# Kernel tuning notes

Hardware: AMD Instinct MI355X
Metric: run time of the kernel (lower is better)

The kernel has to match this reference:

```python
import jax, jax.numpy as jnp
import numpy as np

N = 50000
E = 800000
NODE_DIM = 128
EDGE_DIM = 64


def leaky_relu(x, slope=0.2):
    return jnp.where(x >= 0, x, slope * x)


def setup_inputs() -> dict:
    key = jax.random.key(0)
    ks = jax.random.split(key, 12)
    node_feats = jax.random.normal(ks[0], (N, NODE_DIM), dtype=jnp.float32)
    edge_index = jax.random.randint(ks[1], (2, E), 0, N, dtype=jnp.int64)
    edge_feats = jax.random.normal(ks[2], (E, EDGE_DIM), dtype=jnp.float32)
    # msg_mlp: Linear(node+edge -> node), LeakyReLU(0.2), Linear(node -> node)
    s1 = 1.0 / np.sqrt(NODE_DIM + EDGE_DIM)
    s2 = 1.0 / np.sqrt(NODE_DIM)
    s3 = 1.0 / np.sqrt(2 * NODE_DIM)
    msg_w1 = jax.random.uniform(ks[3], (NODE_DIM + EDGE_DIM, NODE_DIM), jnp.float32, -s1, s1)
    msg_b1 = jax.random.uniform(ks[4], (NODE_DIM,), jnp.float32, -s1, s1)
    msg_w2 = jax.random.uniform(ks[5], (NODE_DIM, NODE_DIM), jnp.float32, -s2, s2)
    msg_b2 = jax.random.uniform(ks[6], (NODE_DIM,), jnp.float32, -s2, s2)
    # update_mlp: Linear(2*node -> node), LeakyReLU(0.2), Linear(node -> node)
    upd_w1 = jax.random.uniform(ks[7], (2 * NODE_DIM, NODE_DIM), jnp.float32, -s3, s3)
    upd_b1 = jax.random.uniform(ks[8], (NODE_DIM,), jnp.float32, -s3, s3)
    upd_w2 = jax.random.uniform(ks[9], (NODE_DIM, NODE_DIM), jnp.float32, -s2, s2)
    upd_b2 = jax.random.uniform(ks[10], (NODE_DIM,), jnp.float32, -s2, s2)
    return {
        "node_feats": node_feats,
        "edge_feats": edge_feats,
        "msg_w1": msg_w1, "msg_b1": msg_b1, "msg_w2": msg_w2, "msg_b2": msg_b2,
        "upd_w1": upd_w1, "upd_b1": upd_b1, "upd_w2": upd_w2, "upd_b2": upd_b2,
        "edge_index": edge_index,
    }


def reference(node_feats, edge_feats, msg_w1, msg_b1, msg_w2, msg_b2,
              upd_w1, upd_b1, upd_w2, upd_b2, edge_index):
    src = edge_index[0]
    dst = edge_index[1]
    # gather neighbor features, concat with edge features: (E, node+edge)
    msg_input = jnp.concatenate([node_feats[dst], edge_feats], axis=1)
    h = leaky_relu(msg_input @ msg_w1 + msg_b1)
    messages = h @ msg_w2 + msg_b2                       # (E, node_dim)
    # scatter-add messages to source nodes
    aggregated = jax.ops.segment_sum(messages, src, num_segments=node_feats.shape[0])
    update_input = jnp.concatenate([node_feats, aggregated], axis=1)  # (N, 2*node_dim)
    h2 = leaky_relu(update_input @ upd_w1 + upd_b1)
    return h2 @ upd_w2 + upd_b2                          # (N, node_dim)
```

## Files before the change

### kernel.cpp

```cpp
#include <hip/hip_runtime.h>
#include <hip/hip_bf16.h>

#define NNODES 50000
#define NEDGES 800000
#define NDIM   128
#define EDIM   64
#define K1     192
#define K2     256
#define NB     196
#define TPB_E  4

#define KPA 136
#define KPU 264

typedef __attribute__((ext_vector_type(8))) short bf16x8;
typedef __attribute__((ext_vector_type(4))) short bf16x4;
typedef __attribute__((ext_vector_type(4))) float f32x4;

__device__ inline short f2bf(float f) {
  union { float f; unsigned u; } v; v.f = f;
  unsigned r = v.u + 0x7FFFu + ((v.u >> 16) & 1u);
  return (short)(r >> 16);
}

__device__ inline bf16x4 pack4(float4 v) {
  bf16x4 p;
  p[0] = f2bf(v.x); p[1] = f2bf(v.y); p[2] = f2bf(v.z); p[3] = f2bf(v.w);
  return p;
}

__device__ inline void wg_barrier_lds() {
  asm volatile("s_waitcnt lgkmcnt(0)" ::: "memory");
  __builtin_amdgcn_s_barrier();
  asm volatile("" ::: "memory");
}

__global__ __launch_bounds__(256) void cvt_kernel(const float* __restrict__ src,
                                                  short* __restrict__ dst, int n) {
  int i = (blockIdx.x * 256 + threadIdx.x) * 4;
  if (i < n) {
    float4 v = *(const float4*)(src + i);
    *(bf16x4*)(dst + i) = pack4(v);
  }
}

__global__ __launch_bounds__(256) void wt_all_kernel(const float* __restrict__ w1,
                                                     const float* __restrict__ w2,
                                                     const float* __restrict__ u1,
                                                     const float* __restrict__ u2,
                                                     short* __restrict__ w1t,
                                                     short* __restrict__ w2t,
                                                     short* __restrict__ u1t,
                                                     short* __restrict__ u2t) {
  int i = blockIdx.x * 256 + threadIdx.x;
  const int A0 = K1 * 128;
  const int A1 = A0 + 128 * 128;
  const int A2 = A1 + K2 * 128;
  const int A3 = A2 + 128 * 128;
  if (i < A0) {
    int j = i, k = j >> 7, n = j & 127;
    w1t[n * K1 + k] = f2bf(w1[j]);
  } else if (i < A1) {
    int j = i - A0, k = j >> 7, n = j & 127;
    w2t[n * NDIM + k] = f2bf(w2[j]);
  } else if (i < A2) {
    int j = i - A1, k = j >> 7, n = j & 127;
    u1t[n * K2 + k] = f2bf(u1[j]);
  } else if (i < A3) {
    int j = i - A2, k = j >> 7, n = j & 127;
    u2t[n * NDIM + k] = f2bf(u2[j]);
  }
}

__global__ __launch_bounds__(256) void hist_kernel(const int* __restrict__ eidx,
                                                   int* __restrict__ cnt) {
  int i = blockIdx.x * 256 + threadIdx.x;
  if (i < NEDGES) atomicAdd(&cnt[eidx[i]], 1);
}

__global__ __launch_bounds__(256) void scan_reduce_kernel(const int* __restrict__ cnt,
                                                          int* __restrict__ bsum) {
  __shared__ int sh[256];
  int tid = threadIdx.x;
  int i = blockIdx.x * 256 + tid;
  sh[tid] = (i < NNODES) ? cnt[i] : 0;
  __syncthreads();
#pragma unroll
  for (int off = 128; off > 0; off >>= 1) {
    if (tid < off) sh[tid] += sh[tid + off];
    __syncthreads();
  }
  if (tid == 0) bsum[blockIdx.x] = sh[0];
}

__global__ __launch_bounds__(256) void scan_top_kernel(const int* __restrict__ bsum,
                                                       int* __restrict__ bscan) {
  __shared__ int sh[256];
  int tid = threadIdx.x;
  int v = (tid < NB) ? bsum[tid] : 0;
  sh[tid] = v;
  __syncthreads();
#pragma unroll
  for (int off = 1; off < 256; off <<= 1) {
    int t = (tid >= off) ? sh[tid - off] : 0;
    __syncthreads();
    sh[tid] += t;
    __syncthreads();
  }
  bscan[tid] = sh[tid] - v;
}

__global__ __launch_bounds__(256) void scan_down_kernel(int* __restrict__ cnt,
                                                        const int* __restrict__ bscan,
                                                        int* __restrict__ row_ptr) {
  __shared__ int sh[256];
  int tid = threadIdx.x;
  int i = blockIdx.x * 256 + tid;
  int v = (i < NNODES) ? cnt[i] : 0;
  sh[tid] = v;
  __syncthreads();
#pragma unroll
  for (int off = 1; off < 256; off <<= 1) {
    int t = (tid >= off) ? sh[tid - off] : 0;
    __syncthreads();
    sh[tid] += t;
    __syncthreads();
  }
  if (i < NNODES) {
    row_ptr[i] = bscan[blockIdx.x] + (sh[tid] - v);
    cnt[i] = 0;
  }
}

__global__ __launch_bounds__(256) void permute_kernel(const int* __restrict__ eidx,
                                                      const int* __restrict__ row_ptr,
                                                      int* __restrict__ cnt,
                                                      int4* __restrict__ s_edges) {
  int e = blockIdx.x * 256 + threadIdx.x;
  if (e < NEDGES) {
    int s = eidx[e];
    int d = eidx[NEDGES + e];
    int pos = row_ptr[s] + atomicAdd(&cnt[s], 1);
    s_edges[pos] = make_int4(s, d, e, 0);
  }
}

__global__ __launch_bounds__(256, 3) void edge_kernel(const short* __restrict__ nf_bf,
                                                      const float* __restrict__ edge_feats,
                                                      const int4* __restrict__ s_edges,
                                                      const short* __restrict__ w1t,
                                                      const float* __restrict__ b1,
                                                      float* __restrict__ hagg) {
  __shared__ __align__(16) short XN[2][64 * 128];
  __shared__ __align__(16) short XE[64 * 64];
  __shared__ int srcs[64];

  const int tid = threadIdx.x;
  const int lane = tid & 63;
  const int wv = tid >> 6;
  const int m16 = lane & 15;
  const int quad = lane >> 4;
  const int r = tid >> 2, q = tid & 3;
  const int rx = r & 7;
  const int mx = m16 & 7;

  const int e0 = blockIdx.x * (64 * TPB_E);

  float bias[2];
#pragma unroll
  for (int nt = 0; nt < 2; ++nt) bias[nt] = b1[wv * 32 + nt * 16 + m16];

  bf16x8 bfrag[6][2];
#pragma unroll
  for (int ks = 0; ks < 6; ++ks)
#pragma unroll
    for (int nt = 0; nt < 2; ++nt)
      bfrag[ks][nt] = *(const bf16x8*)(w1t + (wv * 32 + nt * 16 + m16) * K1 + ks * 32 + quad * 8);

  int4 rec = s_edges[e0 + r];
  bf16x8 pn[4];
  float4 pe[4];
  {
    const bf16x8* np = (const bf16x8*)(nf_bf + (size_t)rec.y * NDIM) + q * 4;
#pragma unroll
    for (int j = 0; j < 4; ++j) pn[j] = np[j];
    const float4* ep = (const float4*)(edge_feats + (size_t)rec.z * EDIM) + q * 4;
#pragma unroll
    for (int j = 0; j < 4; ++j) pe[j] = ep[j];
  }

  for (int t = 0; t < TPB_E; ++t) {
    short* xn = XN[t & 1];

    {
      short* rowp = xn + r * 128;
#pragma unroll
      for (int j = 0; j < 4; ++j)
        *(bf16x8*)(rowp + (((q * 4 + j) ^ rx) << 3)) = pn[j];
      bf16x4 c0 = pack4(pe[0]), c1 = pack4(pe[1]), c2 = pack4(pe[2]), c3 = pack4(pe[3]);
      bf16x8 p0, p1;
      p0[0]=c0[0]; p0[1]=c0[1]; p0[2]=c0[2]; p0[3]=c0[3];
      p0[4]=c1[0]; p0[5]=c1[1]; p0[6]=c1[2]; p0[7]=c1[3];
      p1[0]=c2[0]; p1[1]=c2[1]; p1[2]=c2[2]; p1[3]=c2[3];
      p1[4]=c3[0]; p1[5]=c3[1]; p1[6]=c3[2]; p1[7]=c3[3];
      short* erow = XE + r * 64;
      *(bf16x8*)(erow + (((q * 2 + 0) ^ rx) << 3)) = p0;
      *(bf16x8*)(erow + (((q * 2 + 1) ^ rx) << 3)) = p1;
      if (q == 0) srcs[r] = rec.x;
    }
    __syncthreads();

    if (t + 1 < TPB_E) {
      rec = s_edges[e0 + (t + 1) * 64 + r];
      const bf16x8* np = (const bf16x8*)(nf_bf + (size_t)rec.y * NDIM) + q * 4;
#pragma unroll
      for (int j = 0; j < 4; ++j) pn[j] = np[j];
      const float4* ep = (const float4*)(edge_feats + (size_t)rec.z * EDIM) + q * 4;
#pragma unroll
      for (int j = 0; j < 4; ++j) pe[j] = ep[j];
    }

    f32x4 acc[4][2];
#pragma unroll
    for (int mt = 0; mt < 4; ++mt)
#pragma unroll
      for (int nt = 0; nt < 2; ++nt) acc[mt][nt] = (f32x4){0.f, 0.f, 0.f, 0.f};
#pragma unroll
    for (int ks = 0; ks < 4; ++ks) {
#pragma unroll
      for (int mt = 0; mt < 4; ++mt) {
        bf16x8 a = *(const bf16x8*)(xn + (mt * 16 + m16) * 128 + (((ks * 4 + quad) ^ mx) << 3));
#pragma unroll
        for (int nt = 0; nt < 2; ++nt)
          acc[mt][nt] = __builtin_amdgcn_mfma_f32_16x16x32_bf16(a, bfrag[ks][nt], acc[mt][nt], 0, 0, 0);
      }
    }
#pragma unroll
    for (int ks = 4; ks < 6; ++ks) {
#pragma unroll
      for (int mt = 0; mt < 4; ++mt) {
        bf16x8 a = *(const bf16x8*)(XE + (mt * 16 + m16) * 64 + ((((ks - 4) * 4 + quad) ^ mx) << 3));
#pragma unroll
        for (int nt = 0; nt < 2; ++nt)
          acc[mt][nt] = __builtin_amdgcn_mfma_f32_16x16x32_bf16(a, bfrag[ks][nt], acc[mt][nt], 0, 0, 0);
      }
    }
    wg_barrier_lds();

    float* M = (float*)xn;
#pragma unroll
    for (int h = 0; h < 2; ++h) {
#pragma unroll
      for (int nt = 0; nt < 2; ++nt) {
        const int col = wv * 32 + nt * 16 + m16;
        const float bb = bias[nt];
#pragma unroll
        for (int mt2 = 0; mt2 < 2; ++mt2) {
          const int mt = h * 2 + mt2;
#pragma unroll
          for (int i = 0; i < 4; ++i) {
            float v = acc[mt][nt][i] + bb;
            v = v >= 0.f ? v : 0.2f * v;
            M[(mt2 * 16 + quad * 4 + i) * 128 + col] = v;
          }
        }
      }
      wg_barrier_lds();
      {
        const int c = tid & 127;
        const int lr0 = (tid >> 7) * 16;
        const int g0 = h * 32 + lr0;
        float a = M[lr0 * 128 + c];
        int prev = srcs[g0];
#pragma unroll 4
        for (int rr = 1; rr < 16; ++rr) {
          int s = srcs[g0 + rr];
          float v = M[(lr0 + rr) * 128 + c];
          if (s != prev) {
            atomicAdd(&hagg[(size_t)prev * NDIM + c], a);
            a = v;
            prev = s;
          } else {
            a += v;
          }
        }
        atomicAdd(&hagg[(size_t)prev * NDIM + c], a);
      }
      wg_barrier_lds();
    }
  }
}

__global__ __launch_bounds__(256) void node_kernel(const short* __restrict__ nf_bf,
                                                   const float* __restrict__ hagg,
                                                   const int* __restrict__ degc,
                                                   const short* __restrict__ w2t,
                                                   const float* __restrict__ b2,
                                                   const short* __restrict__ u1t,
                                                   const float* __restrict__ ub1,
                                                   const short* __restrict__ u2t,
                                                   const float* __restrict__ ub2,
                                                   float* __restrict__ out) {
  __shared__ __align__(16) short AGH[32 * KPA];
  __shared__ __align__(16) short XU[32 * KPU];
  __shared__ float degs[32];

  const int tid = threadIdx.x;
  const int n0 = blockIdx.x * 32;

  if (tid < 32) {
    int node = n0 + tid;
    degs[tid] = (node < NNODES) ? (float)degc[node] : 0.f;
  }
  {
    int r = tid >> 3, q = tid & 7;
    int node = n0 + r; if (node >= NNODES) node = NNODES - 1;
    const float4* hp = (const float4*)(hagg + (size_t)node * NDIM) + q * 4;
    const bf16x8* xp = (const bf16x8*)(nf_bf + (size_t)node * NDIM) + q * 2;
    short* ap = AGH + r * KPA + q * 16;
    short* xq = XU + r * KPU + q * 16;
#pragma unroll
    for (int j = 0; j < 4; ++j) *(bf16x4*)(ap + j * 4) = pack4(hp[j]);
#pragma unroll
    for (int j = 0; j < 2; ++j) *(bf16x8*)(xq + j * 8) = xp[j];
  }
  __syncthreads();

  const int lane = tid & 63;
  const int wv = tid >> 6;
  const int m16 = lane & 15;
  const int quad = lane >> 4;

  f32x4 acc[2][2];

#pragma unroll
  for (int mt = 0; mt < 2; ++mt)
#pragma unroll
    for (int nt = 0; nt < 2; ++nt)
      acc[mt][nt] = (f32x4){0.f, 0.f, 0.f, 0.f};
#pragma unroll
  for (int ks = 0; ks < 4; ++ks) {
    const int k0 = ks * 32 + quad * 8;
    bf16x8 b[2];
#pragma unroll
    for (int nt = 0; nt < 2; ++nt) {
      int n = wv * 32 + nt * 16 + m16;
      b[nt] = *(const bf16x8*)(w2t + n * NDIM + k0);
    }
#pragma unroll
    for (int mt = 0; mt < 2; ++mt) {
      bf16x8 a = *(const bf16x8*)(AGH + (mt * 16 + m16) * KPA + k0);
#pragma unroll
      for (int nt = 0; nt < 2; ++nt)
        acc[mt][nt] = __builtin_amdgcn_mfma_f32_16x16x32_bf16(a, b[nt], acc[mt][nt], 0, 0, 0);
    }
  }
#pragma unroll
  for (int nt = 0; nt < 2; ++nt) {
    int col = wv * 32 + nt * 16 + m16;
    float bb = b2[col];
#pragma unroll
    for (int mt = 0; mt < 2; ++mt) {
#pragma unroll
      for (int i = 0; i < 4; ++i) {
        int row = mt * 16 + quad * 4 + i;
        float v = acc[mt][nt][i] + degs[row] * bb;
        XU[row * KPU + NDIM + col] = f2bf(v);
      }
    }
  }
  __syncthreads();

#pragma unroll
  for (int mt = 0; mt < 2; ++mt)
#pragma unroll
    for (int nt = 0; nt < 2; ++nt)
      acc[mt][nt] = (f32x4){0.f, 0.f, 0.f, 0.f};
#pragma unroll
  for (int ks = 0; ks < 8; ++ks) {
    const int k0 = ks * 32 + quad * 8;
    bf16x8 b[2];
#pragma unroll
    for (int nt = 0; nt < 2; ++nt) {
      int n = wv * 32 + nt * 16 + m16;
      b[nt] = *(const bf16x8*)(u1t + n * K2 + k0);
    }
#pragma unroll
    for (int mt = 0; mt < 2; ++mt) {
      bf16x8 a = *(const bf16x8*)(XU + (mt * 16 + m16) * KPU + k0);
#pragma unroll
      for (int nt = 0; nt < 2; ++nt)
        acc[mt][nt] = __builtin_amdgcn_mfma_f32_16x16x32_bf16(a, b[nt], acc[mt][nt], 0, 0, 0);
    }
  }
  __syncthreads();
#pragma unroll
  for (int nt = 0; nt < 2; ++nt) {
    int col = wv * 32 + nt * 16 + m16;
    float bb = ub1[col];
#pragma unroll
    for (int mt = 0; mt < 2; ++mt) {
#pragma unroll
      for (int i = 0; i < 4; ++i) {
        int row = mt * 16 + quad * 4 + i;
        float v = acc[mt][nt][i] + bb;
        v = v >= 0.f ? v : 0.2f * v;
        AGH[row * KPA + col] = f2bf(v);
      }
    }
  }
  __syncthreads();

#pragma unroll
  for (int mt = 0; mt < 2; ++mt)
#pragma unroll
    for (int nt = 0; nt < 2; ++nt)
      acc[mt][nt] = (f32x4){0.f, 0.f, 0.f, 0.f};
#pragma unroll
  for (int ks = 0; ks < 4; ++ks) {
    const int k0 = ks * 32 + quad * 8;
    bf16x8 b[2];
#pragma unroll
    for (int nt = 0; nt < 2; ++nt) {
      int n = wv * 32 + nt * 16 + m16;
      b[nt] = *(const bf16x8*)(u2t + n * NDIM + k0);
    }
#pragma unroll
    for (int mt = 0; mt < 2; ++mt) {
      bf16x8 a = *(const bf16x8*)(AGH + (mt * 16 + m16) * KPA + k0);
#pragma unroll
      for (int nt = 0; nt < 2; ++nt)
        acc[mt][nt] = __builtin_amdgcn_mfma_f32_16x16x32_bf16(a, b[nt], acc[mt][nt], 0, 0, 0);
    }
  }
#pragma unroll
  for (int nt = 0; nt < 2; ++nt) {
    int col = wv * 32 + nt * 16 + m16;
    float bb = ub2[col];
#pragma unroll
    for (int mt = 0; mt < 2; ++mt) {
#pragma unroll
      for (int i = 0; i < 4; ++i) {
        int row = mt * 16 + quad * 4 + i;
        int node = n0 + row;
        if (node < NNODES)
          out[(size_t)node * NDIM + col] = acc[mt][nt][i] + bb;
      }
    }
  }
}

extern "C" void kernel_launch(void* const* d_in, const int* in_sizes, int n_in,
                              void* d_out, int out_size, void* d_ws, size_t ws_size,
                              hipStream_t stream) {
  const float* node_feats = (const float*)d_in[0];
  const float* edge_feats = (const float*)d_in[1];
  const float* msg_w1 = (const float*)d_in[2];
  const float* msg_b1 = (const float*)d_in[3];
  const float* msg_w2 = (const float*)d_in[4];
  const float* msg_b2 = (const float*)d_in[5];
  const float* upd_w1 = (const float*)d_in[6];
  const float* upd_b1 = (const float*)d_in[7];
  const float* upd_w2 = (const float*)d_in[8];
  const float* upd_b2 = (const float*)d_in[9];
  const int* eidx = (const int*)d_in[10];

  float* hagg   = (float*)d_ws;
  int* cnt      = (int*)(hagg + (size_t)NNODES * NDIM);
  int* row_ptr  = cnt + NNODES;
  int* bsum     = row_ptr + NNODES;
  int* bscan    = bsum + 256;
  int4* s_edges = (int4*)(bscan + 256);
  short* w1t    = (short*)(s_edges + NEDGES);
  short* w2t    = w1t + 128 * K1;
  short* u1t    = w2t + 128 * 128;
  short* u2t    = u1t + 128 * K2;
  short* nf_bf  = u2t + 128 * 128;

  hipMemsetAsync(d_ws, 0, (size_t)(NNODES * NDIM + NNODES) * sizeof(float), stream);

  cvt_kernel<<<(NNODES * NDIM / 4 + 255) / 256, 256, 0, stream>>>(node_feats, nf_bf,
                                                                  NNODES * NDIM);
  wt_all_kernel<<<(90112 + 255) / 256, 256, 0, stream>>>(msg_w1, msg_w2, upd_w1, upd_w2,
                                                         w1t, w2t, u1t, u2t);

  hist_kernel<<<NEDGES / 256, 256, 0, stream>>>(eidx, cnt);
  scan_reduce_kernel<<<NB, 256, 0, stream>>>(cnt, bsum);
  scan_top_kernel<<<1, 256, 0, stream>>>(bsum, bscan);
  scan_down_kernel<<<NB, 256, 0, stream>>>(cnt, bscan, row_ptr);
  permute_kernel<<<NEDGES / 256, 256, 0, stream>>>(eidx, row_ptr, cnt, s_edges);

  edge_kernel<<<NEDGES / (64 * TPB_E), 256, 0, stream>>>(nf_bf, edge_feats, s_edges,
                                                         w1t, msg_b1, hagg);
  node_kernel<<<(NNODES + 31) / 32, 256, 0, stream>>>(nf_bf, hagg, cnt,
                                                      w2t, msg_b2, u1t, upd_b1,
                                                      u2t, upd_b2, (float*)d_out);
}
```

Baseline: 507.3 us.

## Merge prep kernels and shrink edge-kernel LDS to raise occupancy

Fuses the node-feature conversion, weight transpose and degree histogram into one prep launch, cutting two kernel launches. The edge kernel drops its double-buffered LDS and reuses a single padded region for inputs and the message staging tile. The padded stride of 130 floats is meant to reduce bank conflicts, and the launch bound is raised to 4 blocks per CU. Each tile now stages all 64 rows at once, with one barrier pair instead of two halves. Losing the double buffer may add serialisation between tiles, and the tighter launch bound may cause register spills.

```diff
diff --git a/kernel.cpp b/kernel.cpp
--- a/kernel.cpp
+++ b/kernel.cpp
@@ -9,6 +9,7 @@
 #define K2     256
 #define NB     196
 #define TPB_E  4
+#define MSTR   130
 
 #define KPA 136
 #define KPU 264
@@ -35,47 +36,46 @@
   asm volatile("" ::: "memory");
 }
 
-__global__ __launch_bounds__(256) void cvt_kernel(const float* __restrict__ src,
-                                                  short* __restrict__ dst, int n) {
-  int i = (blockIdx.x * 256 + threadIdx.x) * 4;
-  if (i < n) {
-    float4 v = *(const float4*)(src + i);
-    *(bf16x4*)(dst + i) = pack4(v);
-  }
-}
-
-__global__ __launch_bounds__(256) void wt_all_kernel(const float* __restrict__ w1,
-                                                     const float* __restrict__ w2,
-                                                     const float* __restrict__ u1,
-                                                     const float* __restrict__ u2,
-                                                     short* __restrict__ w1t,
-                                                     short* __restrict__ w2t,
-                                                     short* __restrict__ u1t,
-                                                     short* __restrict__ u2t) {
-  int i = blockIdx.x * 256 + threadIdx.x;
-  const int A0 = K1 * 128;
-  const int A1 = A0 + 128 * 128;
-  const int A2 = A1 + K2 * 128;
-  const int A3 = A2 + 128 * 128;
-  if (i < A0) {
-    int j = i, k = j >> 7, n = j & 127;
-    w1t[n * K1 + k] = f2bf(w1[j]);
-  } else if (i < A1) {
-    int j = i - A0, k = j >> 7, n = j & 127;
-    w2t[n * NDIM + k] = f2bf(w2[j]);
-  } else if (i < A2) {
-    int j = i - A1, k = j >> 7, n = j & 127;
-    u1t[n * K2 + k] = f2bf(u1[j]);
-  } else if (i < A3) {
-    int j = i - A2, k = j >> 7, n = j & 127;
-    u2t[n * NDIM + k] = f2bf(u2[j]);
-  }
-}
-
-__global__ __launch_bounds__(256) void hist_kernel(const int* __restrict__ eidx,
+__global__ __launch_bounds__(256) void prep_kernel(const float* __restrict__ nf,
+                                                   short* __restrict__ nf_bf,
+                                                   const float* __restrict__ w1,
+                                                   const float* __restrict__ w2,
+                                                   const float* __restrict__ u1,
+                                                   const float* __restrict__ u2,
+                                                   short* __restrict__ w1t,
+                                                   short* __restrict__ w2t,
+                                                   short* __restrict__ u1t,
+                                                   short* __restrict__ u2t,
+                                                   const int* __restrict__ eidx,
                                                    int* __restrict__ cnt) {
-  int i = blockIdx.x * 256 + threadIdx.x;
-  if (i < NEDGES) atomicAdd(&cnt[eidx[i]], 1);
+  const int b = blockIdx.x;
+  const int tid = threadIdx.x;
+  if (b < 6250) {
+    int i = (b * 256 + tid) * 4;
+    float4 v = *(const float4*)(nf + i);
+    *(bf16x4*)(nf_bf + i) = pack4(v);
+  } else if (b < 6602) {
+    int i = (b - 6250) * 256 + tid;
+    const int A0 = K1 * 128;
+    const int A1 = A0 + 128 * 128;
+    const int A2 = A1 + K2 * 128;
+    if (i < A0) {
+      int j = i, k = j >> 7, n = j & 127;
+      w1t[n * K1 + k] = f2bf(w1[j]);
+    } else if (i < A1) {
+      int j = i - A0, k = j >> 7, n = j & 127;
+      w2t[n * NDIM + k] = f2bf(w2[j]);
+    } else if (i < A2) {
+      int j = i - A1, k = j >> 7, n = j & 127;
+      u1t[n * K2 + k] = f2bf(u1[j]);
+    } else {
+      int j = i - A2, k = j >> 7, n = j & 127;
+      u2t[n * NDIM + k] = f2bf(u2[j]);
+    }
+  } else {
+    int e = (b - 6602) * 256 + tid;
+    atomicAdd(&cnt[eidx[e]], 1);
+  }
 }
 
 __global__ __launch_bounds__(256) void scan_reduce_kernel(const int* __restrict__ cnt,
@@ -145,15 +145,18 @@
   }
 }
 
-__global__ __launch_bounds__(256, 3) void edge_kernel(const short* __restrict__ nf_bf,
+__global__ __launch_bounds__(256, 4) void edge_kernel(const short* __restrict__ nf_bf,
                                                       const float* __restrict__ edge_feats,
                                                       const int4* __restrict__ s_edges,
                                                       const short* __restrict__ w1t,
                                                       const float* __restrict__ b1,
                                                       float* __restrict__ hagg) {
-  __shared__ __align__(16) short XN[2][64 * 128];
-  __shared__ __align__(16) short XE[64 * 64];
+  __shared__ __align__(16) char SH[64 * MSTR * 4];
   __shared__ int srcs[64];
+
+  short* X  = (short*)SH;
+  short* XE = (short*)(SH + 16384);
+  float* M  = (float*)SH;
 
   const int tid = threadIdx.x;
   const int lane = tid & 63;
@@ -190,10 +193,8 @@
   }
 
   for (int t = 0; t < TPB_E; ++t) {
-    short* xn = XN[t & 1];
-
     {
-      short* rowp = xn + r * 128;
+      short* rowp = X + r * 128;
 #pragma unroll
       for (int j = 0; j < 4; ++j)
         *(bf16x8*)(rowp + (((q * 4 + j) ^ rx) << 3)) = pn[j];
@@ -229,7 +230,7 @@
     for (int ks = 0; ks < 4; ++ks) {
 #pragma unroll
       for (int mt = 0; mt < 4; ++mt) {
-        bf16x8 a = *(const bf16x8*)(xn + (mt * 16 + m16) * 128 + (((ks * 4 + quad) ^ mx) << 3));
+        bf16x8 a = *(const bf16x8*)(X + (mt * 16 + m16) * 128 + (((ks * 4 + quad) ^ mx) << 3));
 #pragma unroll
         for (int nt = 0; nt < 2; ++nt)
           acc[mt][nt] = __builtin_amdgcn_mfma_f32_16x16x32_bf16(a, bfrag[ks][nt], acc[mt][nt], 0, 0, 0);
@@ -247,35 +248,34 @@
     }
     wg_barrier_lds();
 
-    float* M = (float*)xn;
-#pragma unroll
-    for (int h = 0; h < 2; ++h) {
-#pragma unroll
-      for (int nt = 0; nt < 2; ++nt) {
-        const int col = wv * 32 + nt * 16 + m16;
-        const float bb = bias[nt];
-#pragma unroll
-        for (int mt2 = 0; mt2 < 2; ++mt2) {
-          const int mt = h * 2 + mt2;
-#pragma unroll
-          for (int i = 0; i < 4; ++i) {
-            float v = acc[mt][nt][i] + bb;
-            v = v >= 0.f ? v : 0.2f * v;
-            M[(mt2 * 16 + quad * 4 + i) * 128 + col] = v;
-          }
+#pragma unroll
+    for (int nt = 0; nt < 2; ++nt) {
+      const int col = wv * 32 + nt * 16 + m16;
+      const float bb = bias[nt];
+#pragma unroll
+      for (int mt = 0; mt < 4; ++mt) {
+#pragma unroll
+        for (int i = 0; i < 4; ++i) {
+          float v = acc[mt][nt][i] + bb;
+          v = v >= 0.f ? v : 0.2f * v;
+          M[(mt * 16 + quad * 4 + i) * MSTR + col] = v;
         }
       }
-      wg_barrier_lds();
-      {
-        const int c = tid & 127;
-        const int lr0 = (tid >> 7) * 16;
-        const int g0 = h * 32 + lr0;
-        float a = M[lr0 * 128 + c];
-        int prev = srcs[g0];
+    }
+    wg_barrier_lds();
+
+    {
+      const int c = tid & 127;
+      const int sb = (tid >> 7) * 16;
+#pragma unroll
+      for (int half = 0; half < 2; ++half) {
+        const int lr0 = sb + half * 32;
+        float a = M[lr0 * MSTR + c];
+        int prev = srcs[lr0];
 #pragma unroll 4
         for (int rr = 1; rr < 16; ++rr) {
-          int s = srcs[g0 + rr];
-          float v = M[(lr0 + rr) * 128 + c];
+          int s = srcs[lr0 + rr];
+          float v = M[(lr0 + rr) * MSTR + c];
           if (s != prev) {
             atomicAdd(&hagg[(size_t)prev * NDIM + c], a);
             a = v;
@@ -286,8 +286,8 @@
         }
         atomicAdd(&hagg[(size_t)prev * NDIM + c], a);
       }
-      wg_barrier_lds();
-    }
+    }
+    wg_barrier_lds();
   }
 }
 
@@ -479,12 +479,10 @@
 
   hipMemsetAsync(d_ws, 0, (size_t)(NNODES * NDIM + NNODES) * sizeof(float), stream);
 
-  cvt_kernel<<<(NNODES * NDIM / 4 + 255) / 256, 256, 0, stream>>>(node_feats, nf_bf,
-                                                                  NNODES * NDIM);
-  wt_all_kernel<<<(90112 + 255) / 256, 256, 0, stream>>>(msg_w1, msg_w2, upd_w1, upd_w2,
-                                                         w1t, w2t, u1t, u2t);
-
-  hist_kernel<<<NEDGES / 256, 256, 0, stream>>>(eidx, cnt);
+  prep_kernel<<<9727, 256, 0, stream>>>(node_feats, nf_bf,
+                                        msg_w1, msg_w2, upd_w1, upd_w2,
+                                        w1t, w2t, u1t, u2t, eidx, cnt);
+
   scan_reduce_kernel<<<NB, 256, 0, stream>>>(cnt, bsum);
   scan_top_kernel<<<1, 256, 0, stream>>>(bsum, bscan);
   scan_down_kernel<<<NB, 256, 0, stream>>>(cnt, bscan, row_ptr);
```

Result: slower. 637.6 us (+25.7%).
